# Kernel optimization log

Hardware: AMD Instinct MI355X
Metric: run time of the kernel (lower is better)

The kernel has to match this reference:

```python
import jax, jax.numpy as jnp
import numpy as np

B, G, D, H, KD = 32, 512, 128, 4, 32  # batch, graph, embed_dim, n_heads, key_dim=embed//heads
NORM = 1.0 / np.sqrt(KD).astype(np.float32)  # MultiHeadCompat norm_factor = 1/sqrt(key_dim)


def _uniform(k, shape, fan):
    s = 1.0 / np.sqrt(fan).astype(np.float32)
    return jax.random.uniform(k, shape, jnp.float32, -s, s)


def setup_inputs() -> dict:
    key = jax.random.key(0)
    ks = jax.random.split(key, 16)
    inp = {
        "h": jax.random.normal(ks[0], (B, G, D), jnp.float32),
        "pos_pickup": jax.random.randint(ks[1], (B,), 0, G),
        "pos_delivery": jax.random.randint(ks[2], (B,), 0, G),
        "rec": jax.random.randint(ks[3], (B, G), 0, G),
        # compater_insert1 / compater_insert2 projections: (n_heads, input_dim, key_dim)
        "Wq1": _uniform(ks[4], (H, D, KD), KD),
        "Wk1": _uniform(ks[5], (H, D, KD), KD),
        "Wq2": _uniform(ks[6], (H, D, KD), KD),
        "Wk2": _uniform(ks[7], (H, D, KD), KD),
        # agg MLP(16, 32, 32, 1); stored as (in, out) so y = x @ W + b
        "fc1_w": _uniform(ks[8], (16, 32), 16),
        "fc1_b": _uniform(ks[9], (32,), 32),
        "fc2_w": _uniform(ks[10], (32, 32), 32),
        "fc2_b": _uniform(ks[11], (32,), 32),
        "fc3_w": _uniform(ks[12], (32, 1), 32),
        "fc3_b": _uniform(ks[13], (1,), 1),
    }
    return inp


def _compat(qv, hh, Wq, Wk):
    # qv: (B, D) single query node; hh: (B, G, D)
    Q = jnp.einsum('bd,hdk->bhk', qv, Wq)       # (B, H, K)
    K = jnp.einsum('bgd,hdk->bhgk', hh, Wk)     # (B, H, G, K)
    return NORM * jnp.einsum('bhk,bhgk->bgh', Q, K)  # (B, G, H)


def reference(h, pos_pickup, pos_delivery, rec, Wq1, Wk1, Wq2, Wk2,
              fc1_w, fc1_b, fc2_w, fc2_b, fc3_w, fc3_b):
    b, g, d = h.shape
    ar = jnp.arange(b)
    h_pickup = h[ar, pos_pickup]      # (B, D)
    h_delivery = h[ar, pos_delivery]  # (B, D)
    h_neighbour = jnp.take_along_axis(h, rec[:, :, None], axis=1)  # (B, G, D)

    shp = (b, g, g, 4)
    c_pp = jnp.broadcast_to(_compat(h_pickup, h, Wq1, Wk1)[:, :, None, :], shp)
    c_po = jnp.broadcast_to(_compat(h_pickup, h_neighbour, Wq2, Wk2)[:, :, None, :], shp)
    c_dp = jnp.broadcast_to(_compat(h_delivery, h, Wq1, Wk1)[:, None, :, :], shp)
    c_do = jnp.broadcast_to(_compat(h_delivery, h_neighbour, Wq2, Wk2)[:, None, :, :], shp)
    x = jnp.concatenate([c_pp, c_po, c_dp, c_do], axis=-1)  # (B, G, G, 16)

    # agg MLP (dropout p=0.05 is identity at inference)
    x = jax.nn.relu(x @ fc1_w + fc1_b)
    x = jax.nn.relu(x @ fc2_w + fc2_b)
    return (x @ fc3_w + fc3_b)[..., 0]  # (B, G, G)
```

## Files before the change

### kernel.cpp

```cpp
#include <hip/hip_runtime.h>


#define B 32
#define G 512
#define D 128
#define NH 4
#define KD 32
#define NORMF 0.17677669529663687f

#define WS_APQ 0
#define WS_APO 16384
#define WS_ADP 32768
#define WS_ADO 49152
#define WS_P16H 131072
#define WS_Q16H 655360

typedef float v16f __attribute__((ext_vector_type(16)));
typedef _Float16 v8h __attribute__((ext_vector_type(8)));
typedef _Float16 h2 __attribute__((ext_vector_type(2)));

union Q8 {
  uint4 u;
  h2 h[4];
  v8h v;
};

__global__ __launch_bounds__(128) void precompute_A(
    const float* __restrict__ h, const int* __restrict__ pp, const int* __restrict__ pd,
    const float* __restrict__ Wq1, const float* __restrict__ Wk1,
    const float* __restrict__ Wq2, const float* __restrict__ Wk2,
    float* __restrict__ ws) {
  const int b = blockIdx.x;
  const int t = threadIdx.x;
  __shared__ float hp[D], hd[D];
  __shared__ float q1p[NH * KD], q2p[NH * KD], q1d[NH * KD], q2d[NH * KD];

  hp[t] = h[(b * G + pp[b]) * D + t];
  hd[t] = h[(b * G + pd[b]) * D + t];
  __syncthreads();

  {
    const int hh = t >> 5, k = t & 31;
    const float* wq1 = Wq1 + hh * D * KD + k;
    const float* wq2 = Wq2 + hh * D * KD + k;
    float s1p = 0.f, s2p = 0.f, s1d = 0.f, s2d = 0.f;
    for (int d = 0; d < D; ++d) {
      const float w1 = wq1[d * KD], w2 = wq2[d * KD];
      const float xp = hp[d], xd = hd[d];
      s1p = fmaf(xp, w1, s1p);
      s2p = fmaf(xp, w2, s2p);
      s1d = fmaf(xd, w1, s1d);
      s2d = fmaf(xd, w2, s2d);
    }
    q1p[t] = s1p; q2p[t] = s2p; q1d[t] = s1d; q2d[t] = s2d;
  }
  __syncthreads();

  const int d = t;
  for (int hh = 0; hh < NH; ++hh) {
    const float* wk1 = Wk1 + hh * D * KD + d * KD;
    const float* wk2 = Wk2 + hh * D * KD + d * KD;
    float apq = 0.f, apo = 0.f, adp = 0.f, ado = 0.f;
#pragma unroll
    for (int k = 0; k < KD; ++k) {
      const float w1 = wk1[k], w2 = wk2[k];
      apq = fmaf(q1p[hh * 32 + k], w1, apq);
      adp = fmaf(q1d[hh * 32 + k], w1, adp);
      apo = fmaf(q2p[hh * 32 + k], w2, apo);
      ado = fmaf(q2d[hh * 32 + k], w2, ado);
    }
    const int o = b * (NH * D) + hh * D + d;
    ws[WS_APQ + o] = NORMF * apq;
    ws[WS_APO + o] = NORMF * apo;
    ws[WS_ADP + o] = NORMF * adp;
    ws[WS_ADO + o] = NORMF * ado;
  }
}

__global__ __launch_bounds__(256) void compute_PQ(
    const float* __restrict__ h, const int* __restrict__ rec,
    const float* __restrict__ fc1_w, const float* __restrict__ fc1_b,
    float* __restrict__ ws) {
  const int bx = blockIdx.x;
  const int b = bx >> 3, g0 = (bx & 7) * 64;
  const int t = threadIdx.x;
  const int gl = t & 63;
  const int hh = __builtin_amdgcn_readfirstlane(t >> 6);
  const int g = g0 + gl;

  __shared__ float sc[64][17];
  __shared__ float sout[64][33];

  const float* Apq = ws + WS_APQ + (b * NH + hh) * D;
  const float* Apo = ws + WS_APO + (b * NH + hh) * D;
  const float* Adp = ws + WS_ADP + (b * NH + hh) * D;
  const float* Ado = ws + WS_ADO + (b * NH + hh) * D;
  const float4* hg4 = (const float4*)(h + ((size_t)b * G + g) * D);
  const float4* hn4 = (const float4*)(h + ((size_t)b * G + rec[b * G + g]) * D);

  float cpp = 0.f, cpo = 0.f, cdp = 0.f, cdo = 0.f;
#pragma unroll 4
  for (int d4 = 0; d4 < 32; ++d4) {
    const float4 x = hg4[d4], y = hn4[d4];
    const float4 a1 = *(const float4*)(Apq + d4 * 4);
    const float4 a2 = *(const float4*)(Apo + d4 * 4);
    const float4 a3 = *(const float4*)(Adp + d4 * 4);
    const float4 a4 = *(const float4*)(Ado + d4 * 4);
    cpp = fmaf(x.x, a1.x, fmaf(x.y, a1.y, fmaf(x.z, a1.z, fmaf(x.w, a1.w, cpp))));
    cpo = fmaf(y.x, a2.x, fmaf(y.y, a2.y, fmaf(y.z, a2.z, fmaf(y.w, a2.w, cpo))));
    cdp = fmaf(x.x, a3.x, fmaf(x.y, a3.y, fmaf(x.z, a3.z, fmaf(x.w, a3.w, cdp))));
    cdo = fmaf(y.x, a4.x, fmaf(y.y, a4.y, fmaf(y.z, a4.z, fmaf(y.w, a4.w, cdo))));
  }
  sc[gl][hh] = cpp; sc[gl][4 + hh] = cpo; sc[gl][8 + hh] = cdp; sc[gl][12 + hh] = cdo;
  __syncthreads();

  float u[16];
#pragma unroll
  for (int i = 0; i < 16; ++i) u[i] = sc[gl][i];

  float pv[8], qv[8];
#pragma unroll
  for (int jj = 0; jj < 8; ++jj) {
    const int j = hh * 8 + jj;
    float p = 0.f, q = fc1_b[j];
#pragma unroll
    for (int i = 0; i < 8; ++i) {
      p = fmaf(u[i], fc1_w[i * 32 + j], p);
      q = fmaf(u[8 + i], fc1_w[(8 + i) * 32 + j], q);
    }
    pv[jj] = p; qv[jj] = q;
  }

#pragma unroll
  for (int jj = 0; jj < 8; ++jj) sout[gl][hh * 8 + jj] = pv[jj];
  __syncthreads();
  {
    unsigned* dst = (unsigned*)((unsigned short*)ws + WS_P16H) +
                    ((size_t)b * G + g0) * 16;
#pragma unroll
    for (int i = t; i < 1024; i += 256) {
      const int row = i >> 4, c0 = (2 * i) & 31;
      __fp16 __attribute__((ext_vector_type(2))) pk =
          __builtin_amdgcn_cvt_pkrtz(sout[row][c0], sout[row][c0 + 1]);
      dst[i] = *(const unsigned*)&pk;
    }
  }
  __syncthreads();
#pragma unroll
  for (int jj = 0; jj < 8; ++jj) sout[gl][hh * 8 + jj] = qv[jj];
  __syncthreads();
  {
    unsigned* dst = (unsigned*)((unsigned short*)ws + WS_Q16H) +
                    ((size_t)b * G + g0) * 16;
#pragma unroll
    for (int i = t; i < 1024; i += 256) {
      const int row = i >> 4, c0 = (2 * i) & 31;
      __fp16 __attribute__((ext_vector_type(2))) pk =
          __builtin_amdgcn_cvt_pkrtz(sout[row][c0], sout[row][c0 + 1]);
      dst[i] = *(const unsigned*)&pk;
    }
  }
}

__global__ __launch_bounds__(256) void mlp_pairs(
    const float* __restrict__ ws,
    const float* __restrict__ fc2_w, const float* __restrict__ fc2_b,
    const float* __restrict__ fc3_w, const float* __restrict__ fc3_b,
    float* __restrict__ out) {
  const int b = blockIdx.z;
  const int g1_0 = blockIdx.y * 16;
  const int g2_0 = blockIdx.x * 256;
  const int t = threadIdx.x;
  const int w = t >> 6, l = t & 63;
  const int col = l & 31;
  const int half = l >> 5;
  const int kb = half * 8;

  __shared__ __align__(16) unsigned short sPh[16 * 32];
  {
    const unsigned* Psrc = (const unsigned*)((const unsigned short*)ws + WS_P16H) +
                           ((size_t)b * G + g1_0) * 16;
    ((unsigned*)sPh)[t] = Psrc[t];
  }

  v8h A0, A1;
#pragma unroll
  for (int j = 0; j < 8; ++j) {
    A0[j] = (_Float16)fc2_w[(kb + j) * 32 + col];
    A1[j] = (_Float16)fc2_w[(16 + kb + j) * 32 + col];
  }
  v16f biasC;
  float w3v[16];
#pragma unroll
  for (int r = 0; r < 16; ++r) {
    const int n = (r & 3) + 8 * (r >> 2) + 4 * half;
    biasC[r] = fc2_b[n];
    w3v[r]   = fc3_w[n];
  }
  const float b3 = fc3_b[0];

  Q8 q0[2], q1[2];
#pragma unroll
  for (int c = 0; c < 2; ++c) {
    const unsigned short* qp = (const unsigned short*)ws + WS_Q16H +
        ((size_t)b * G + g2_0 + (2 * w + c) * 32 + col) * 32;
    q0[c].u = *(const uint4*)(qp + kb);
    q1[c].u = *(const uint4*)(qp + 16 + kb);
  }
  __syncthreads();

  const h2 zero = {(_Float16)0.0f, (_Float16)0.0f};
  const size_t outbase = ((size_t)b * G + g1_0) * G + g2_0 + w * 64;
  for (int g1 = 0; g1 < 16; ++g1) {
    const Q8 p0 = *(const Q8*)(sPh + g1 * 32 + kb);
    const Q8 p1 = *(const Q8*)(sPh + g1 * 32 + 16 + kb);

    float s[2];
#pragma unroll
    for (int c = 0; c < 2; ++c) {
      Q8 B0, B1;
#pragma unroll
      for (int i = 0; i < 4; ++i) {
        B0.h[i] = __builtin_elementwise_max(p0.h[i] + q0[c].h[i], zero);
        B1.h[i] = __builtin_elementwise_max(p1.h[i] + q1[c].h[i], zero);
      }
      v16f acc = __builtin_amdgcn_mfma_f32_32x32x16_f16(A0, B0.v, biasC, 0, 0, 0);
      acc = __builtin_amdgcn_mfma_f32_32x32x16_f16(A1, B1.v, acc, 0, 0, 0);

      float e0 = 0.f, e1 = 0.f;
#pragma unroll
      for (int r = 0; r < 16; r += 2) {
        e0 = fmaf(fmaxf(acc[r], 0.f), w3v[r], e0);
        e1 = fmaf(fmaxf(acc[r + 1], 0.f), w3v[r + 1], e1);
      }
      s[c] = e0 + e1;
    }
    const float t0 = s[0] + __shfl_xor(s[0], 32);
    const float t1 = s[1] + __shfl_xor(s[1], 32);
    out[outbase + (size_t)g1 * G + l] = (l < 32 ? t0 : t1) + b3;
  }
}

extern "C" void kernel_launch(void* const* d_in, const int* in_sizes, int n_in,
                              void* d_out, int out_size, void* d_ws, size_t ws_size,
                              hipStream_t stream) {
  const float* h     = (const float*)d_in[0];
  const int*   pp    = (const int*)d_in[1];
  const int*   pd    = (const int*)d_in[2];
  const int*   rec   = (const int*)d_in[3];
  const float* Wq1   = (const float*)d_in[4];
  const float* Wk1   = (const float*)d_in[5];
  const float* Wq2   = (const float*)d_in[6];
  const float* Wk2   = (const float*)d_in[7];
  const float* fc1_w = (const float*)d_in[8];
  const float* fc1_b = (const float*)d_in[9];
  const float* fc2_w = (const float*)d_in[10];
  const float* fc2_b = (const float*)d_in[11];
  const float* fc3_w = (const float*)d_in[12];
  const float* fc3_b = (const float*)d_in[13];
  float* out = (float*)d_out;
  float* ws  = (float*)d_ws;

  precompute_A<<<dim3(B), dim3(128), 0, stream>>>(h, pp, pd, Wq1, Wk1, Wq2, Wk2, ws);
  compute_PQ<<<dim3(256), dim3(256), 0, stream>>>(h, rec, fc1_w, fc1_b, ws);
  mlp_pairs<<<dim3(2, 32, 32), dim3(256), 0, stream>>>(
      ws, fc2_w, fc2_b, fc3_w, fc3_b, out);
}
```

Baseline: 152.2 us.

## Fuse A-precompute into PQ kernel and retile pair MLP for coalesced stores

The per-batch A-vector precompute is merged into the PQ kernel: each block recomputes the projected query vectors for its batch into shared memory instead of reading them from workspace, which removes one launch and a global round trip at the cost of redundant compute across the 8 blocks per batch. The pair MLP now gives each wave 32 g2 columns and processes two g1 rows per iteration, so each 64-lane store covers two output rows. The grid doubles in x, and each block handles 128 g2 columns instead of 256.

```diff
diff --git a/kernel.cpp b/kernel.cpp
--- a/kernel.cpp
+++ b/kernel.cpp
@@ -8,38 +8,50 @@
 #define KD 32
 #define NORMF 0.17677669529663687f
 
-#define WS_APQ 0
-#define WS_APO 16384
-#define WS_ADP 32768
-#define WS_ADO 49152
 #define WS_P16H 131072
 #define WS_Q16H 655360
 
 typedef float v16f __attribute__((ext_vector_type(16)));
 typedef _Float16 v8h __attribute__((ext_vector_type(8)));
-typedef _Float16 h2 __attribute__((ext_vector_type(2)));
-
-union Q8 {
-  uint4 u;
-  h2 h[4];
-  v8h v;
-};
-
-__global__ __launch_bounds__(128) void precompute_A(
-    const float* __restrict__ h, const int* __restrict__ pp, const int* __restrict__ pd,
+typedef _Float16 h2v __attribute__((ext_vector_type(2)));
+
+struct HQ { h2v h[4]; };
+
+__device__ __forceinline__ v8h relu_add(const HQ& p, const HQ& q) {
+  const h2v z = {(_Float16)0.0f, (_Float16)0.0f};
+  HQ r;
+#pragma unroll
+  for (int i = 0; i < 4; ++i)
+    r.h[i] = __builtin_elementwise_max(p.h[i] + q.h[i], z);
+  return __builtin_bit_cast(v8h, r);
+}
+
+__global__ __launch_bounds__(256) void stage01(
+    const float* __restrict__ h, const int* __restrict__ pp,
+    const int* __restrict__ pd, const int* __restrict__ rec,
     const float* __restrict__ Wq1, const float* __restrict__ Wk1,
     const float* __restrict__ Wq2, const float* __restrict__ Wk2,
+    const float* __restrict__ fc1_w, const float* __restrict__ fc1_b,
     float* __restrict__ ws) {
-  const int b = blockIdx.x;
+  const int bx = blockIdx.x;
+  const int b = bx >> 3, g0 = (bx & 7) * 64;
   const int t = threadIdx.x;
+
   __shared__ float hp[D], hd[D];
-  __shared__ float q1p[NH * KD], q2p[NH * KD], q1d[NH * KD], q2d[NH * KD];
-
-  hp[t] = h[(b * G + pp[b]) * D + t];
-  hd[t] = h[(b * G + pd[b]) * D + t];
-  __syncthreads();
-
-  {
+  __shared__ float qq[4][NH * KD];
+  __shared__ float sA[4][NH][D];
+  __shared__ float sc[64][17];
+  __shared__ float sout[64][33];
+
+  if (t < 128) {
+    hp[t] = h[((size_t)b * G + pp[b]) * D + t];
+  } else {
+    const int u = t - 128;
+    hd[u] = h[((size_t)b * G + pd[b]) * D + u];
+  }
+  __syncthreads();
+
+  if (t < 128) {
     const int hh = t >> 5, k = t & 31;
     const float* wq1 = Wq1 + hh * D * KD + k;
     const float* wq2 = Wq2 + hh * D * KD + k;
@@ -52,49 +64,37 @@
       s1d = fmaf(xd, w1, s1d);
       s2d = fmaf(xd, w2, s2d);
     }
-    q1p[t] = s1p; q2p[t] = s2p; q1d[t] = s1d; q2d[t] = s2d;
-  }
-  __syncthreads();
-
-  const int d = t;
-  for (int hh = 0; hh < NH; ++hh) {
-    const float* wk1 = Wk1 + hh * D * KD + d * KD;
-    const float* wk2 = Wk2 + hh * D * KD + d * KD;
-    float apq = 0.f, apo = 0.f, adp = 0.f, ado = 0.f;
-#pragma unroll
-    for (int k = 0; k < KD; ++k) {
-      const float w1 = wk1[k], w2 = wk2[k];
-      apq = fmaf(q1p[hh * 32 + k], w1, apq);
-      adp = fmaf(q1d[hh * 32 + k], w1, adp);
-      apo = fmaf(q2p[hh * 32 + k], w2, apo);
-      ado = fmaf(q2d[hh * 32 + k], w2, ado);
-    }
-    const int o = b * (NH * D) + hh * D + d;
-    ws[WS_APQ + o] = NORMF * apq;
-    ws[WS_APO + o] = NORMF * apo;
-    ws[WS_ADP + o] = NORMF * adp;
-    ws[WS_ADO + o] = NORMF * ado;
-  }
-}
-
-__global__ __launch_bounds__(256) void compute_PQ(
-    const float* __restrict__ h, const int* __restrict__ rec,
-    const float* __restrict__ fc1_w, const float* __restrict__ fc1_b,
-    float* __restrict__ ws) {
-  const int bx = blockIdx.x;
-  const int b = bx >> 3, g0 = (bx & 7) * 64;
-  const int t = threadIdx.x;
+    qq[0][t] = s1p; qq[1][t] = s2p; qq[2][t] = s1d; qq[3][t] = s2d;
+  }
+  __syncthreads();
+
+  {
+    const int d = t & 127;
+    const int h0 = (t >> 7) * 2;
+#pragma unroll
+    for (int hh = h0; hh < h0 + 2; ++hh) {
+      const float* wk1 = Wk1 + hh * D * KD + d * KD;
+      const float* wk2 = Wk2 + hh * D * KD + d * KD;
+      float apq = 0.f, apo = 0.f, adp = 0.f, ado = 0.f;
+#pragma unroll
+      for (int k = 0; k < KD; ++k) {
+        const float w1 = wk1[k], w2 = wk2[k];
+        apq = fmaf(qq[0][hh * 32 + k], w1, apq);
+        adp = fmaf(qq[2][hh * 32 + k], w1, adp);
+        apo = fmaf(qq[1][hh * 32 + k], w2, apo);
+        ado = fmaf(qq[3][hh * 32 + k], w2, ado);
+      }
+      sA[0][hh][d] = NORMF * apq;
+      sA[1][hh][d] = NORMF * apo;
+      sA[2][hh][d] = NORMF * adp;
+      sA[3][hh][d] = NORMF * ado;
+    }
+  }
+  __syncthreads();
+
   const int gl = t & 63;
   const int hh = __builtin_amdgcn_readfirstlane(t >> 6);
   const int g = g0 + gl;
-
-  __shared__ float sc[64][17];
-  __shared__ float sout[64][33];
-
-  const float* Apq = ws + WS_APQ + (b * NH + hh) * D;
-  const float* Apo = ws + WS_APO + (b * NH + hh) * D;
-  const float* Adp = ws + WS_ADP + (b * NH + hh) * D;
-  const float* Ado = ws + WS_ADO + (b * NH + hh) * D;
   const float4* hg4 = (const float4*)(h + ((size_t)b * G + g) * D);
   const float4* hn4 = (const float4*)(h + ((size_t)b * G + rec[b * G + g]) * D);
 
@@ -102,10 +102,10 @@
 #pragma unroll 4
   for (int d4 = 0; d4 < 32; ++d4) {
     const float4 x = hg4[d4], y = hn4[d4];
-    const float4 a1 = *(const float4*)(Apq + d4 * 4);
-    const float4 a2 = *(const float4*)(Apo + d4 * 4);
-    const float4 a3 = *(const float4*)(Adp + d4 * 4);
-    const float4 a4 = *(const float4*)(Ado + d4 * 4);
+    const float4 a1 = *(const float4*)&sA[0][hh][4 * d4];
+    const float4 a2 = *(const float4*)&sA[1][hh][4 * d4];
+    const float4 a3 = *(const float4*)&sA[2][hh][4 * d4];
+    const float4 a4 = *(const float4*)&sA[3][hh][4 * d4];
     cpp = fmaf(x.x, a1.x, fmaf(x.y, a1.y, fmaf(x.z, a1.z, fmaf(x.w, a1.w, cpp))));
     cpo = fmaf(y.x, a2.x, fmaf(y.y, a2.y, fmaf(y.z, a2.z, fmaf(y.w, a2.w, cpo))));
     cdp = fmaf(x.x, a3.x, fmaf(x.y, a3.y, fmaf(x.z, a3.z, fmaf(x.w, a3.w, cdp))));
@@ -169,7 +169,7 @@
     float* __restrict__ out) {
   const int b = blockIdx.z;
   const int g1_0 = blockIdx.y * 16;
-  const int g2_0 = blockIdx.x * 256;
+  const int g2_0 = blockIdx.x * 128;
   const int t = threadIdx.x;
   const int w = t >> 6, l = t & 63;
   const int col = l & 31;
@@ -199,45 +199,46 @@
   }
   const float b3 = fc3_b[0];
 
-  Q8 q0[2], q1[2];
-#pragma unroll
-  for (int c = 0; c < 2; ++c) {
+  HQ qlo, qhi;
+  {
     const unsigned short* qp = (const unsigned short*)ws + WS_Q16H +
-        ((size_t)b * G + g2_0 + (2 * w + c) * 32 + col) * 32;
-    q0[c].u = *(const uint4*)(qp + kb);
-    q1[c].u = *(const uint4*)(qp + 16 + kb);
-  }
-  __syncthreads();
-
-  const h2 zero = {(_Float16)0.0f, (_Float16)0.0f};
-  const size_t outbase = ((size_t)b * G + g1_0) * G + g2_0 + w * 64;
-  for (int g1 = 0; g1 < 16; ++g1) {
-    const Q8 p0 = *(const Q8*)(sPh + g1 * 32 + kb);
-    const Q8 p1 = *(const Q8*)(sPh + g1 * 32 + 16 + kb);
-
-    float s[2];
-#pragma unroll
-    for (int c = 0; c < 2; ++c) {
-      Q8 B0, B1;
-#pragma unroll
-      for (int i = 0; i < 4; ++i) {
-        B0.h[i] = __builtin_elementwise_max(p0.h[i] + q0[c].h[i], zero);
-        B1.h[i] = __builtin_elementwise_max(p1.h[i] + q1[c].h[i], zero);
-      }
-      v16f acc = __builtin_amdgcn_mfma_f32_32x32x16_f16(A0, B0.v, biasC, 0, 0, 0);
-      acc = __builtin_amdgcn_mfma_f32_32x32x16_f16(A1, B1.v, acc, 0, 0, 0);
-
-      float e0 = 0.f, e1 = 0.f;
-#pragma unroll
-      for (int r = 0; r < 16; r += 2) {
-        e0 = fmaf(fmaxf(acc[r], 0.f), w3v[r], e0);
-        e1 = fmaf(fmaxf(acc[r + 1], 0.f), w3v[r + 1], e1);
-      }
-      s[c] = e0 + e1;
-    }
-    const float t0 = s[0] + __shfl_xor(s[0], 32);
-    const float t1 = s[1] + __shfl_xor(s[1], 32);
-    out[outbase + (size_t)g1 * G + l] = (l < 32 ? t0 : t1) + b3;
+        ((size_t)b * G + g2_0 + w * 32 + col) * 32;
+    qlo = __builtin_bit_cast(HQ, *(const uint4*)(qp + kb));
+    qhi = __builtin_bit_cast(HQ, *(const uint4*)(qp + 16 + kb));
+  }
+  __syncthreads();
+
+  float* op = out + (((size_t)b * G + g1_0 + half) * G) + g2_0 + w * 32 + col;
+#pragma unroll
+  for (int i = 0; i < 8; ++i) {
+    const int ra = 2 * i, rb = 2 * i + 1;
+    const HQ palo = __builtin_bit_cast(HQ, *(const uint4*)(sPh + ra * 32 + kb));
+    const HQ pahi = __builtin_bit_cast(HQ, *(const uint4*)(sPh + ra * 32 + 16 + kb));
+    const HQ pblo = __builtin_bit_cast(HQ, *(const uint4*)(sPh + rb * 32 + kb));
+    const HQ pbhi = __builtin_bit_cast(HQ, *(const uint4*)(sPh + rb * 32 + 16 + kb));
+
+    const v8h Balo = relu_add(palo, qlo);
+    const v8h Bahi = relu_add(pahi, qhi);
+    const v8h Bblo = relu_add(pblo, qlo);
+    const v8h Bbhi = relu_add(pbhi, qhi);
+
+    v16f acca = __builtin_amdgcn_mfma_f32_32x32x16_f16(A0, Balo, biasC, 0, 0, 0);
+    v16f accb = __builtin_amdgcn_mfma_f32_32x32x16_f16(A0, Bblo, biasC, 0, 0, 0);
+    acca = __builtin_amdgcn_mfma_f32_32x32x16_f16(A1, Bahi, acca, 0, 0, 0);
+    accb = __builtin_amdgcn_mfma_f32_32x32x16_f16(A1, Bbhi, accb, 0, 0, 0);
+
+    float a0 = 0.f, a1 = 0.f, b0 = 0.f, b1 = 0.f;
+#pragma unroll
+    for (int r = 0; r < 16; r += 2) {
+      a0 = fmaf(fmaxf(acca[r], 0.f), w3v[r], a0);
+      a1 = fmaf(fmaxf(acca[r + 1], 0.f), w3v[r + 1], a1);
+      b0 = fmaf(fmaxf(accb[r], 0.f), w3v[r], b0);
+      b1 = fmaf(fmaxf(accb[r + 1], 0.f), w3v[r + 1], b1);
+    }
+    float sa = a0 + a1, sb = b0 + b1;
+    sa += __shfl_xor(sa, 32);
+    sb += __shfl_xor(sb, 32);
+    op[(size_t)ra * G] = (half ? sb : sa) + b3;
   }
 }
 
@@ -261,8 +262,8 @@
   float* out = (float*)d_out;
   float* ws  = (float*)d_ws;
 
-  precompute_A<<<dim3(B), dim3(128), 0, stream>>>(h, pp, pd, Wq1, Wk1, Wq2, Wk2, ws);
-  compute_PQ<<<dim3(256), dim3(256), 0, stream>>>(h, rec, fc1_w, fc1_b, ws);
-  mlp_pairs<<<dim3(2, 32, 32), dim3(256), 0, stream>>>(
+  stage01<<<dim3(256), dim3(256), 0, stream>>>(
+      h, pp, pd, rec, Wq1, Wk1, Wq2, Wk2, fc1_w, fc1_b, ws);
+  mlp_pairs<<<dim3(4, 32, 32), dim3(256), 0, stream>>>(
       ws, fc2_w, fc2_b, fc3_w, fc3_b, out);
 }
```

Result: faster. 148.9 us (-2.1%).
